# Optimization experiments

Measured on AMD Instinct MI355X. Metric: run time of the kernel, lower is better.

## Reference

```python
import jax, jax.numpy as jnp
import numpy as np

K = 3  # kernel_size
P = K // 2


def setup_inputs() -> dict:
    key = jax.random.key(0)
    k1, k2 = jax.random.split(key)
    x = jax.random.normal(k1, (8, 64, 256, 256), dtype=jnp.float32)
    alpha = jnp.full((1, 64, 1, 1), 0.1, dtype=jnp.float32)
    return {"x": x, "alpha": alpha}


def reference(x, alpha):
    # Equivalent to F.unfold(x, K, padding=P) -> abs-diff from center -> sum over K*K -> residual.
    b, c, h, w = x.shape
    xp = jnp.pad(x, ((0, 0), (0, 0), (P, P), (P, P)))  # zero padding, same as F.unfold
    diff_sum = jnp.zeros_like(x)
    for di in range(K):
        for dj in range(K):
            neighbor = xp[:, :, di:di + h, dj:dj + w]
            diff_sum = diff_sum + jnp.abs(x - neighbor)
    return x + alpha * diff_sum
```

## Files before the change

### kernel.cpp

```cpp
#include <hip/hip_runtime.h>


constexpr int H = 256;
constexpr int W = 256;
constexpr int C = 64;

__global__ __launch_bounds__(256) void adc_kernel(
    const float* __restrict__ x,
    const float* __restrict__ alpha,
    float* __restrict__ out)
{
    const long tid = (long)blockIdx.x * blockDim.x + threadIdx.x;
    const long row = tid >> 6;
    const int  g   = (int)(tid & 63);
    const int  y   = (int)(row & (H - 1));
    const long bc  = row >> 8;
    const int  c   = (int)(bc & (C - 1));

    const float* img  = x   + bc * (long)(H * W);
    float*       outp = out + bc * (long)(H * W);
    const float  a    = alpha[c];
    const int    w0   = g * 4;

    float v[3][6];
#pragma unroll
    for (int r = 0; r < 3; ++r) {
        const int yy = y + r - 1;
        if (yy < 0 || yy >= H) {
#pragma unroll
            for (int j = 0; j < 6; ++j) v[r][j] = 0.f;
        } else {
            const float* rowp = img + (long)yy * W + w0;
            const float4 ctr = *(const float4*)rowp;
            v[r][1] = ctr.x; v[r][2] = ctr.y; v[r][3] = ctr.z; v[r][4] = ctr.w;
            v[r][0] = (w0 > 0)     ? rowp[-1] : 0.f;
            v[r][5] = (w0 + 4 < W) ? rowp[4]  : 0.f;
        }
    }

    float4 res;
    float* rp = &res.x;
#pragma unroll
    for (int j = 0; j < 4; ++j) {
        const float xc = v[1][j + 1];
        float s = 0.f;
#pragma unroll
        for (int r = 0; r < 3; ++r)
#pragma unroll
            for (int d = 0; d < 3; ++d)
                s += fabsf(xc - v[r][j + d]);
        rp[j] = fmaf(a, s, xc);
    }
    *(float4*)(outp + (long)y * W + w0) = res;
}

extern "C" void kernel_launch(void* const* d_in, const int* in_sizes, int n_in,
                              void* d_out, int out_size, void* d_ws, size_t ws_size,
                              hipStream_t stream)
{
    const float* x     = (const float*)d_in[0];
    const float* alpha = (const float*)d_in[1];
    float*       out   = (float*)d_out;

    const long total_rows    = 8L * C * H;
    const long total_threads = total_rows * (W / 4);
    const int  block = 256;
    const long grid  = (total_threads + block - 1) / block;

    adc_kernel<<<(int)grid, block, 0, stream>>>(x, alpha, out);
}
```

Before: 253.7 us.

## Compute four rows per thread and fetch horizontal halos via wave shuffles

Each wavefront now covers four consecutive output rows of a full 256-wide image row and loads six input rows once, instead of each thread reloading three rows for a single output row. Left and right halo values come from neighbouring lanes via shuffles rather than extra unaligned scalar global loads. This cuts redundant global and cache traffic and memory instruction count, at the cost of more registers per thread and fewer threads in flight.

```diff
diff --git a/kernel.cpp b/kernel.cpp
--- a/kernel.cpp
+++ b/kernel.cpp
@@ -10,48 +10,50 @@
     const float* __restrict__ alpha,
     float* __restrict__ out)
 {
-    const long tid = (long)blockIdx.x * blockDim.x + threadIdx.x;
-    const long row = tid >> 6;
-    const int  g   = (int)(tid & 63);
-    const int  y   = (int)(row & (H - 1));
-    const long bc  = row >> 8;
-    const int  c   = (int)(bc & (C - 1));
+    const int lane = threadIdx.x & 63;
+    const int wave = threadIdx.x >> 6;
+    const long slab = (long)blockIdx.x;
+    const long img  = slab >> 4;
+    const int  s16  = (int)(slab & 15);
+    const int  y0   = s16 * 16 + wave * 4;
+    const int  c    = (int)(img & (C - 1));
 
-    const float* img  = x   + bc * (long)(H * W);
-    float*       outp = out + bc * (long)(H * W);
     const float  a    = alpha[c];
-    const int    w0   = g * 4;
+    const float* imgp = x   + img * (long)(H * W);
+    float*       outp = out + img * (long)(H * W);
+    const int    w0   = lane * 4;
 
-    float v[3][6];
+    float v[6][6];
 #pragma unroll
-    for (int r = 0; r < 3; ++r) {
-        const int yy = y + r - 1;
-        if (yy < 0 || yy >= H) {
-#pragma unroll
-            for (int j = 0; j < 6; ++j) v[r][j] = 0.f;
-        } else {
-            const float* rowp = img + (long)yy * W + w0;
-            const float4 ctr = *(const float4*)rowp;
-            v[r][1] = ctr.x; v[r][2] = ctr.y; v[r][3] = ctr.z; v[r][4] = ctr.w;
-            v[r][0] = (w0 > 0)     ? rowp[-1] : 0.f;
-            v[r][5] = (w0 + 4 < W) ? rowp[4]  : 0.f;
-        }
+    for (int r = 0; r < 6; ++r) {
+        const int yy = y0 + r - 1;
+        float4 ctr = make_float4(0.f, 0.f, 0.f, 0.f);
+        if (yy >= 0 && yy < H)
+            ctr = *(const float4*)(imgp + (long)yy * W + w0);
+        v[r][1] = ctr.x; v[r][2] = ctr.y; v[r][3] = ctr.z; v[r][4] = ctr.w;
+        const float left  = __shfl_up(ctr.w, 1);
+        const float right = __shfl_down(ctr.x, 1);
+        v[r][0] = (lane == 0)  ? 0.f : left;
+        v[r][5] = (lane == 63) ? 0.f : right;
     }
 
-    float4 res;
-    float* rp = &res.x;
 #pragma unroll
-    for (int j = 0; j < 4; ++j) {
-        const float xc = v[1][j + 1];
-        float s = 0.f;
+    for (int o = 0; o < 4; ++o) {
+        float4 res;
+        float* rp = &res.x;
 #pragma unroll
-        for (int r = 0; r < 3; ++r)
+        for (int j = 0; j < 4; ++j) {
+            const float xc = v[o + 1][j + 1];
+            float s = 0.f;
 #pragma unroll
-            for (int d = 0; d < 3; ++d)
-                s += fabsf(xc - v[r][j + d]);
-        rp[j] = fmaf(a, s, xc);
+            for (int r = 0; r < 3; ++r)
+#pragma unroll
+                for (int d = 0; d < 3; ++d)
+                    s += fabsf(xc - v[o + r][j + d]);
+            rp[j] = fmaf(a, s, xc);
+        }
+        *(float4*)(outp + (long)(y0 + o) * W + w0) = res;
     }
-    *(float4*)(outp + (long)y * W + w0) = res;
 }
 
 extern "C" void kernel_launch(void* const* d_in, const int* in_sizes, int n_in,
@@ -62,10 +64,6 @@
     const float* alpha = (const float*)d_in[1];
     float*       out   = (float*)d_out;
 
-    const long total_rows    = 8L * C * H;
-    const long total_threads = total_rows * (W / 4);
-    const int  block = 256;
-    const long grid  = (total_threads + block - 1) / block;
-
-    adc_kernel<<<(int)grid, block, 0, stream>>>(x, alpha, out);
+    const int grid = 8 * C * (H / 16);
+    adc_kernel<<<grid, 256, 0, stream>>>(x, alpha, out);
 }
```

Result: faster. 234.7 us (-7.5%).
